# Performance work log

Hardware: AMD Instinct MI355X
Metric: run time of the kernel (lower is better)

## Reference

```python
import jax, jax.numpy as jnp
import numpy as np

B_SZ, D, H, W = 32, 96, 64, 64
N = 4            # d_state
R = 6            # dt_rank = ceil(96/16)
K = 5            # d_conv
EPS = 1e-9
LOG_EPS = float(np.log(EPS))


def setup_inputs() -> dict:
    key = jax.random.key(0)
    ks = jax.random.split(key, 8)
    x = jax.random.normal(ks[0], (B_SZ, D, H, W), dtype=jnp.float32)
    conv_w = jax.random.normal(ks[1], (D, 1, K, K), dtype=jnp.float32) * (1.0 / K)
    conv_b = jax.random.normal(ks[2], (D,), dtype=jnp.float32) * 0.02
    x_proj_w = jax.random.normal(ks[3], (R + 2 * N, D), dtype=jnp.float32) * (D ** -0.5)
    dt_w = jax.random.uniform(ks[4], (D, R), dtype=jnp.float32, minval=-(R ** -0.5), maxval=R ** -0.5)
    # dt bias init: inverse-softplus of dt ~ U(log 1e-3, log 1e-1)
    dt = jnp.exp(jax.random.uniform(ks[5], (D,), dtype=jnp.float32) * (np.log(0.1) - np.log(0.001)) + np.log(0.001))
    dt = jnp.clip(dt, 1e-4, None)
    dt_b = dt + jnp.log(-jnp.expm1(-dt))
    A_logs = jnp.log(jnp.broadcast_to(jnp.arange(1, N + 1, dtype=jnp.float32), (D, N)))
    Ds = jnp.ones((D,), dtype=jnp.float32)
    return {"x": x, "conv_w": conv_w, "conv_b": conv_b, "x_proj_w": x_proj_w,
            "dt_w": dt_w, "dt_b": dt_b, "A_logs": A_logs, "Ds": Ds}


def _forward(x, conv_w, conv_b, x_proj_w, dt_w, dt_b, A_logs, Ds):
    B, C, h, w = x.shape
    L = h * w
    # depthwise conv2d, padding='same' for odd kernel, + SiLU
    x = jax.lax.conv_general_dilated(
        x, conv_w, window_strides=(1, 1), padding=((K // 2, K // 2), (K // 2, K // 2)),
        dimension_numbers=("NCHW", "OIHW", "NCHW"), feature_group_count=C)
    x = x + conv_b[None, :, None, None]
    x = jax.nn.silu(x)
    xs = x.reshape(B, C, L)                                  # [B, D, L]
    x_dbl = jnp.einsum("kd,bdl->bkl", x_proj_w, xs)          # [B, R+2N, L]
    dts, Bs, Cs = x_dbl[:, :R], x_dbl[:, R:R + N], x_dbl[:, R + N:]
    delta = jax.nn.softplus(jnp.einsum("dr,brl->bdl", dt_w, dts) + dt_b[None, :, None])
    A = -jnp.exp(A_logs)                                     # [D, N]
    # log(dA.clamp(min=EPS)) with dA = exp(delta * A)  ==  max(delta*A, log EPS)
    log_dA = jnp.maximum(delta[:, :, None, :] * A[None, :, :, None], LOG_EPS)  # [B,D,N,L]
    P = jnp.exp(jnp.cumsum(log_dA, axis=-1))                 # [B,D,N,L]
    dB_u = delta[:, :, None, :] * Bs[:, None, :, :] * xs[:, :, None, :]        # [B,D,N,L]
    hs = P * jnp.cumsum(dB_u / jnp.maximum(P, EPS), axis=-1)  # state trajectory
    y = jnp.einsum("bdnl,bnl->bdl", hs, Cs) + xs * Ds[None, :, None]
    return y.reshape(B, C, h, w)


def reference(x, conv_w, conv_b, x_proj_w, dt_w, dt_b, A_logs, Ds):
    return _forward(x, conv_w, conv_b, x_proj_w, dt_w, dt_b, A_logs, Ds)
```

## Files before the change

### kernel.cpp

```cpp
#include <hip/hip_runtime.h>

#define B_SZ 32
#define D_CH 96
#define L_SZ 4096
#define N_ST 4
#define R_RK 6

static __device__ __forceinline__ float softplus_f(float v) {
    return fmaxf(v, 0.0f) + __logf(1.0f + __expf(-fabsf(v)));
}

static __device__ __forceinline__ float exp2_fast(float x) {
#if __has_builtin(__builtin_amdgcn_exp2f)
    return __builtin_amdgcn_exp2f(x);
#else
    return __expf(x * 0.6931471805599453f);
#endif
}

template<int CTRL, int RMASK>
static __device__ __forceinline__ float dpp_add(float v) {
    const int t = __builtin_amdgcn_update_dpp(0, __float_as_int(v),
                                              CTRL, RMASK, 0xf, true);
    return v + __int_as_float(t);
}

static __device__ __forceinline__ float wave_incl_scan(float v) {
    v = dpp_add<0x111, 0xf>(v);
    v = dpp_add<0x112, 0xf>(v);
    v = dpp_add<0x114, 0xf>(v);
    v = dpp_add<0x118, 0xf>(v);
    v = dpp_add<0x142, 0xa>(v);
    v = dpp_add<0x143, 0xc>(v);
    return v;
}

static __device__ __forceinline__ float block_excl_scan(float v, float* slot, int t)
{
    const int lane = t & 63;
    const int wid  = t >> 6;
    const float incl = wave_incl_scan(v);
    if (lane == 63) slot[wid] = incl;
    const float ex = incl - v;
    __syncthreads();
    float wp = 0.0f;
#pragma unroll
    for (int w = 0; w < 7; ++w)
        if (w < wid) wp += slot[w];
    return wp + ex;
}

#define TS 76
__global__ __launch_bounds__(256) void conv_silu_kernel(
    const float* __restrict__ x, const float* __restrict__ conv_w,
    const float* __restrict__ conv_b, float* __restrict__ xs)
{
    __shared__ float tile[68 * TS];
    const int t = threadIdx.x;
    const int bd = blockIdx.x;
    const int d = bd % D_CH;
    const float* img = x + bd * L_SZ;

    float wreg[25];
#pragma unroll
    for (int i = 0; i < 25; ++i) wreg[i] = conv_w[d * 25 + i];
    const float bias = conv_b[d];

    const float4 z4 = make_float4(0.f, 0.f, 0.f, 0.f);
    for (int i = t; i < 268; i += 256) {
        float4* p;
        if (i < 192) {
            const int r = 2 + i / 3;
            const int c = i - (i / 3) * 3;
            const int gw = (c == 0) ? 0 : (c == 1 ? 68 : 72);
            p = (float4*)(tile + r * TS + gw);
        } else {
            const int j = i - 192;
            const int half = j / 19;
            const int c4 = j - half * 19;
            const int r = (half < 2) ? half : 64 + half;
            p = (float4*)(tile + r * TS + c4 * 4);
        }
        *p = z4;
    }
    for (int i = t; i < 1024; i += 256) {
        const int r = i >> 4;
        const int c = (i & 15) << 2;
        const float4 v = *(const float4*)(img + (r << 6) + c);
        *(float4*)(tile + (r + 2) * TS + 4 + c) = v;
    }
    __syncthreads();

    const int hr = t >> 2;
    const int cb = (t & 3) << 4;

    float acc[16];
#pragma unroll
    for (int j = 0; j < 16; ++j) acc[j] = bias;

#pragma unroll
    for (int kh = 0; kh < 5; ++kh) {
        const float* rp = tile + (hr + kh) * TS + cb;
        float r24[24];
#pragma unroll
        for (int q = 0; q < 6; ++q) {
            const float4 v = ((const float4*)rp)[q];
            r24[4*q+0] = v.x; r24[4*q+1] = v.y; r24[4*q+2] = v.z; r24[4*q+3] = v.w;
        }
#pragma unroll
        for (int j = 0; j < 16; ++j)
#pragma unroll
            for (int kw = 0; kw < 5; ++kw)
                acc[j] += wreg[kh * 5 + kw] * r24[j + kw + 2];
    }

    float* out = xs + bd * L_SZ + (hr << 6) + cb;
#pragma unroll
    for (int q = 0; q < 4; ++q) {
        float4 v;
#pragma unroll
        for (int j = 0; j < 4; ++j) {
            const float a = acc[4*q + j];
            const float s = __builtin_amdgcn_rcpf(1.0f + __expf(-a));
            (&v.x)[j] = a * s;
        }
        ((float4*)out)[q] = v;
    }
}

__global__ __launch_bounds__(256) void proj_kernel(
    const float* __restrict__ xs, const float* __restrict__ x_proj_w,
    float* __restrict__ x_dbl)
{
    __shared__ float red[4][14][64];
    const int t = threadIdx.x;
    const int g = t >> 6;
    const int ll = t & 63;
    const int bi = blockIdx.x;
    const int b = bi >> 6;
    const int chunk = bi & 63;
    const int l = (chunk << 6) + ll;
    const int d0 = __builtin_amdgcn_readfirstlane(g * 24);

    const float* xsb = xs + (b * D_CH + d0) * L_SZ + l;
    float acc[14];
#pragma unroll
    for (int k = 0; k < 14; ++k) acc[k] = 0.0f;

#pragma unroll
    for (int dd = 0; dd < 24; ++dd) {
        const float xv = xsb[dd * L_SZ];
#pragma unroll
        for (int k = 0; k < 14; ++k)
            acc[k] += x_proj_w[k * D_CH + d0 + dd] * xv;
    }

#pragma unroll
    for (int k = 0; k < 14; ++k) red[g][k][ll] = acc[k];
    __syncthreads();

    float* outb = x_dbl + b * 14 * L_SZ + (chunk << 6);
    for (int i = t; i < 14 * 64; i += 256) {
        const int k = i >> 6;
        const int c = i & 63;
        outb[k * L_SZ + c] = red[0][k][c] + red[1][k][c] + red[2][k][c] + red[3][k][c];
    }
}

__global__ __launch_bounds__(512, 4) void scan_kernel(
    const float* __restrict__ xs, const float* __restrict__ x_dbl,
    const float* __restrict__ dt_w, const float* __restrict__ dt_b,
    const float* __restrict__ A_logs, const float* __restrict__ Ds,
    float* __restrict__ y)
{
    constexpr float L2EPS = -29.897352853986263f;
    constexpr float L2E   = 1.4426950408889634f;

    __shared__ float slots[8][8];
    const int t = threadIdx.x;
    const int bd = blockIdx.x;
    const int b = bd / D_CH;
    const int d = bd - b * D_CH;
    const int l0 = t * 8;

    const float* xs_row = xs + bd * L_SZ + l0;
    const float* xd = x_dbl + b * 14 * L_SZ + l0;

    float xv[8];
#pragma unroll
    for (int i = 0; i < 2; ++i) {
        const float4 v = ((const float4*)xs_row)[i];
        xv[4*i+0] = v.x; xv[4*i+1] = v.y; xv[4*i+2] = v.z; xv[4*i+3] = v.w;
    }

    const float dtb = dt_b[d];
    float dl[8];
#pragma unroll
    for (int i = 0; i < 8; ++i) dl[i] = dtb;
#pragma unroll
    for (int r = 0; r < R_RK; ++r) {
        const float wr = dt_w[d * R_RK + r];
        const float* row = xd + r * L_SZ;
#pragma unroll
        for (int i = 0; i < 2; ++i) {
            const float4 v = ((const float4*)row)[i];
            dl[4*i+0] += wr * v.x; dl[4*i+1] += wr * v.y;
            dl[4*i+2] += wr * v.z; dl[4*i+3] += wr * v.w;
        }
    }
#pragma unroll
    for (int i = 0; i < 8; ++i) dl[i] = softplus_f(dl[i]);

    const float dsd = Ds[d];
    float dlxv[8], yac[8];
#pragma unroll
    for (int i = 0; i < 8; ++i) { dlxv[i] = dl[i] * xv[i]; yac[i] = xv[i] * dsd; }

    for (int n = 0; n < N_ST; ++n) {
        const float An2 = -__expf(A_logs[d * N_ST + n]) * L2E;

        float SP[8];
        float run = 0.0f;
#pragma unroll
        for (int i = 0; i < 8; ++i) {
            run += fmaxf(dl[i] * An2, L2EPS);
            SP[i] = run;
        }
        const float ex1 = block_excl_scan(run, slots[2*n], t);

        const float* Brow = xd + (R_RK + n) * L_SZ;
        float carr[8];
        float run2 = 0.0f;
#pragma unroll
        for (int i = 0; i < 2; ++i) {
            const float4 v = ((const float4*)Brow)[i];
            const float bb[4] = {v.x, v.y, v.z, v.w};
#pragma unroll
            for (int j = 0; j < 4; ++j) {
                const int idx = 4*i + j;
                const float S = SP[idx] + ex1;
                const float e = exp2_fast(-S);
                const float pinv = fminf(e, 1e9f);
                SP[idx] = __builtin_amdgcn_rcpf(e);
                run2 = fmaf(dlxv[idx] * bb[j], pinv, run2);
                carr[idx] = run2;
            }
        }
        const float ex2 = block_excl_scan(run2, slots[2*n+1], t);

        const float* Crow = xd + (R_RK + N_ST + n) * L_SZ;
#pragma unroll
        for (int i = 0; i < 2; ++i) {
            const float4 v = ((const float4*)Crow)[i];
            const float cc[4] = {v.x, v.y, v.z, v.w};
#pragma unroll
            for (int j = 0; j < 4; ++j) {
                const int idx = 4*i + j;
                yac[idx] = fmaf(SP[idx] * (carr[idx] + ex2), cc[j], yac[idx]);
            }
        }
    }

    float* yrow = y + bd * L_SZ + l0;
#pragma unroll
    for (int i = 0; i < 2; ++i) {
        float4 v;
        v.x = yac[4*i+0]; v.y = yac[4*i+1];
        v.z = yac[4*i+2]; v.w = yac[4*i+3];
        ((float4*)yrow)[i] = v;
    }
}

extern "C" void kernel_launch(void* const* d_in, const int* in_sizes, int n_in,
                              void* d_out, int out_size, void* d_ws, size_t ws_size,
                              hipStream_t stream)
{
    const float* x        = (const float*)d_in[0];
    const float* conv_w   = (const float*)d_in[1];
    const float* conv_b   = (const float*)d_in[2];
    const float* x_proj_w = (const float*)d_in[3];
    const float* dt_w     = (const float*)d_in[4];
    const float* dt_b     = (const float*)d_in[5];
    const float* A_logs   = (const float*)d_in[6];
    const float* Ds       = (const float*)d_in[7];

    float* y     = (float*)d_out;
    float* xs    = y;
    float* x_dbl = (float*)d_ws;

    conv_silu_kernel<<<B_SZ * D_CH, 256, 0, stream>>>(x, conv_w, conv_b, xs);
    proj_kernel<<<B_SZ * 64, 256, 0, stream>>>(xs, x_proj_w, x_dbl);
    scan_kernel<<<B_SZ * D_CH, 512, 0, stream>>>(xs, x_dbl, dt_w, dt_b,
                                                 A_logs, Ds, y);
}
```

Measured before the change: 84.19 us.

## Share one delta prefix scan across states when the log-eps clamp never binds

Adds a fast path that computes a single block-wide inclusive scan of delta, plus a block max of delta. When max(delta)*max(exp(A_log)) shows the log-eps clamp can never trigger, cumsum(delta*A) equals A*cumsum(delta), so each state derives its decay from the shared scan instead of running its own. This cuts the block scans and barriers from eight to five per block. The original per-state path remains as a fallback, at the cost of extra code size and register pressure.

```diff
diff --git a/kernel.cpp b/kernel.cpp
--- a/kernel.cpp
+++ b/kernel.cpp
@@ -23,6 +23,12 @@
     const int t = __builtin_amdgcn_update_dpp(0, __float_as_int(v),
                                               CTRL, RMASK, 0xf, true);
     return v + __int_as_float(t);
+}
+template<int CTRL, int RMASK>
+static __device__ __forceinline__ float dpp_max(float v) {
+    const int t = __builtin_amdgcn_update_dpp(0, __float_as_int(v),
+                                              CTRL, RMASK, 0xf, true);
+    return fmaxf(v, __int_as_float(t));
 }
 
 static __device__ __forceinline__ float wave_incl_scan(float v) {
@@ -32,6 +38,15 @@
     v = dpp_add<0x118, 0xf>(v);
     v = dpp_add<0x142, 0xa>(v);
     v = dpp_add<0x143, 0xc>(v);
+    return v;
+}
+static __device__ __forceinline__ float wave_max_scan(float v) {
+    v = dpp_max<0x111, 0xf>(v);
+    v = dpp_max<0x112, 0xf>(v);
+    v = dpp_max<0x114, 0xf>(v);
+    v = dpp_max<0x118, 0xf>(v);
+    v = dpp_max<0x142, 0xa>(v);
+    v = dpp_max<0x143, 0xc>(v);
     return v;
 }
 
@@ -176,8 +191,11 @@
     constexpr float L2EPS = -29.897352853986263f;
     constexpr float L2E   = 1.4426950408889634f;
 
-    __shared__ float slots[8][8];
-    const int t = threadIdx.x;
+    __shared__ float slots[9][8];
+    __shared__ float mslot[8];
+    const int t    = threadIdx.x;
+    const int lane = t & 63;
+    const int wid  = t >> 6;
     const int bd = blockIdx.x;
     const int b = bd / D_CH;
     const int d = bd - b * D_CH;
@@ -216,47 +234,115 @@
 #pragma unroll
     for (int i = 0; i < 8; ++i) { dlxv[i] = dl[i] * xv[i]; yac[i] = xv[i] * dsd; }
 
-    for (int n = 0; n < N_ST; ++n) {
-        const float An2 = -__expf(A_logs[d * N_ST + n]) * L2E;
-
-        float SP[8];
-        float run = 0.0f;
-#pragma unroll
-        for (int i = 0; i < 8; ++i) {
-            run += fmaxf(dl[i] * An2, L2EPS);
-            SP[i] = run;
-        }
-        const float ex1 = block_excl_scan(run, slots[2*n], t);
-
-        const float* Brow = xd + (R_RK + n) * L_SZ;
-        float carr[8];
-        float run2 = 0.0f;
-#pragma unroll
-        for (int i = 0; i < 2; ++i) {
-            const float4 v = ((const float4*)Brow)[i];
-            const float bb[4] = {v.x, v.y, v.z, v.w};
-#pragma unroll
-            for (int j = 0; j < 4; ++j) {
-                const int idx = 4*i + j;
-                const float S = SP[idx] + ex1;
-                const float e = exp2_fast(-S);
-                const float pinv = fminf(e, 1e9f);
-                SP[idx] = __builtin_amdgcn_rcpf(e);
-                run2 = fmaf(dlxv[idx] * bb[j], pinv, run2);
-                carr[idx] = run2;
-            }
-        }
-        const float ex2 = block_excl_scan(run2, slots[2*n+1], t);
-
-        const float* Crow = xd + (R_RK + N_ST + n) * L_SZ;
-#pragma unroll
-        for (int i = 0; i < 2; ++i) {
-            const float4 v = ((const float4*)Crow)[i];
-            const float cc[4] = {v.x, v.y, v.z, v.w};
-#pragma unroll
-            for (int j = 0; j < 4; ++j) {
-                const int idx = 4*i + j;
-                yac[idx] = fmaf(SP[idx] * (carr[idx] + ex2), cc[j], yac[idx]);
+    float T[8];
+    float rund = 0.0f;
+#pragma unroll
+    for (int i = 0; i < 8; ++i) { rund += dl[i]; T[i] = rund; }
+    float mx = dl[0];
+#pragma unroll
+    for (int i = 1; i < 8; ++i) mx = fmaxf(mx, dl[i]);
+
+    const float incl_d = wave_incl_scan(rund);
+    const float mxw    = wave_max_scan(mx);
+    if (lane == 63) { slots[8][wid] = incl_d; mslot[wid] = mxw; }
+    const float exw_d = incl_d - rund;
+    __syncthreads();
+
+    float wp = 0.0f;
+#pragma unroll
+    for (int w = 0; w < 7; ++w)
+        if (w < wid) wp += slots[8][w];
+    const float exd = wp + exw_d;
+    float bmax = mslot[0];
+#pragma unroll
+    for (int w = 1; w < 8; ++w) bmax = fmaxf(bmax, mslot[w]);
+
+    float amax = 0.0f;
+#pragma unroll
+    for (int n = 0; n < N_ST; ++n)
+        amax = fmaxf(amax, __expf(A_logs[d * N_ST + n]));
+
+    if (bmax * (amax * L2E) <= 29.0f) {
+#pragma unroll
+        for (int i = 0; i < 8; ++i) T[i] += exd;
+
+        for (int n = 0; n < N_ST; ++n) {
+            const float nA = __expf(A_logs[d * N_ST + n]) * L2E;
+
+            const float* Brow = xd + (R_RK + n) * L_SZ;
+            float carr[8], P[8];
+            float run2 = 0.0f;
+#pragma unroll
+            for (int i = 0; i < 2; ++i) {
+                const float4 v = ((const float4*)Brow)[i];
+                const float bb[4] = {v.x, v.y, v.z, v.w};
+#pragma unroll
+                for (int j = 0; j < 4; ++j) {
+                    const int idx = 4*i + j;
+                    const float e = exp2_fast(nA * T[idx]);
+                    const float pinv = fminf(e, 1e9f);
+                    P[idx] = __builtin_amdgcn_rcpf(e);
+                    run2 = fmaf(dlxv[idx] * bb[j], pinv, run2);
+                    carr[idx] = run2;
+                }
+            }
+            const float ex2 = block_excl_scan(run2, slots[4 + n], t);
+
+            const float* Crow = xd + (R_RK + N_ST + n) * L_SZ;
+#pragma unroll
+            for (int i = 0; i < 2; ++i) {
+                const float4 v = ((const float4*)Crow)[i];
+                const float cc[4] = {v.x, v.y, v.z, v.w};
+#pragma unroll
+                for (int j = 0; j < 4; ++j) {
+                    const int idx = 4*i + j;
+                    yac[idx] = fmaf(P[idx] * (carr[idx] + ex2), cc[j], yac[idx]);
+                }
+            }
+        }
+    } else {
+        for (int n = 0; n < N_ST; ++n) {
+            const float An2 = -__expf(A_logs[d * N_ST + n]) * L2E;
+
+            float SP[8];
+            float run = 0.0f;
+#pragma unroll
+            for (int i = 0; i < 8; ++i) {
+                run += fmaxf(dl[i] * An2, L2EPS);
+                SP[i] = run;
+            }
+            const float ex1 = block_excl_scan(run, slots[2*n], t);
+
+            const float* Brow = xd + (R_RK + n) * L_SZ;
+            float carr[8];
+            float run2 = 0.0f;
+#pragma unroll
+            for (int i = 0; i < 2; ++i) {
+                const float4 v = ((const float4*)Brow)[i];
+                const float bb[4] = {v.x, v.y, v.z, v.w};
+#pragma unroll
+                for (int j = 0; j < 4; ++j) {
+                    const int idx = 4*i + j;
+                    const float S = SP[idx] + ex1;
+                    const float e = exp2_fast(-S);
+                    const float pinv = fminf(e, 1e9f);
+                    SP[idx] = __builtin_amdgcn_rcpf(e);
+                    run2 = fmaf(dlxv[idx] * bb[j], pinv, run2);
+                    carr[idx] = run2;
+                }
+            }
+            const float ex2 = block_excl_scan(run2, slots[2*n+1], t);
+
+            const float* Crow = xd + (R_RK + N_ST + n) * L_SZ;
+#pragma unroll
+            for (int i = 0; i < 2; ++i) {
+                const float4 v = ((const float4*)Crow)[i];
+                const float cc[4] = {v.x, v.y, v.z, v.w};
+#pragma unroll
+                for (int j = 0; j < 4; ++j) {
+                    const int idx = 4*i + j;
+                    yac[idx] = fmaf(SP[idx] * (carr[idx] + ex2), cc[j], yac[idx]);
+                }
             }
         }
     }
```

After: 115.1 us. +36.8%, slower.
